# Kernel tuning notes

Hardware: AMD Instinct MI355X
Metric: run time of the kernel (lower is better)

## Reference

```python
import jax, jax.numpy as jnp
import numpy as np


def setup_inputs() -> dict:
    key = jax.random.key(0)
    k1, k2 = jax.random.split(key)
    B, H, S = 16, 512, 1024          # batch, hidden=nd*embed_dim, seqlen
    ND, ED, K = 4, 128, 4096         # nd, embed_dim, num_embed
    inputs = jax.random.normal(k1, (B, H, S), dtype=jnp.float32)
    embeddings = jax.random.normal(k2, (ND, ED, K), dtype=jnp.float32)
    return {"inputs": inputs, "embeddings": embeddings}


def reference(inputs, embeddings):
    # VectorQuant.forward with soft_train=False, gsoftmax=False, EMA=False (VQ-VAE straight-through path)
    commit_cost = 0.25
    B, H, S = inputs.shape
    ND, ED, K = embeddings.shape
    # stack_enc_outputs: (B, H, S) -> (B*S, nd, embed_dim) via contiguous view (C-order reshape)
    enc = inputs.reshape(B * S, ND, ED)
    x2 = jnp.sum(enc * enc, axis=2, keepdims=True)            # (BS, nd, 1)
    e2 = jnp.sum(embeddings * embeddings, axis=1)[None]       # (1, nd, K)
    cross = jnp.einsum('dhk,bdh->bdk', embeddings, enc)       # (BS, nd, K)
    distances = x2 + e2 - 2.0 * cross
    # per-token, per-chunk nearest code
    latents = jnp.argmin(distances, axis=2).T                 # (nd, BS)
    # gather codebook vectors: embeddings[d][:, latents[d]] -> (nd, ED, BS)
    encodings = jnp.take_along_axis(embeddings, latents[:, None, :], axis=2)
    # split_outputs: (nd, ED, B*S) -> (B, H, S) via contiguous view (C-order reshape)
    encodings = encodings.reshape(B, H, S)
    # straight-through estimator
    output = inputs + jax.lax.stop_gradient(encodings) - jax.lax.stop_gradient(inputs)
    commit_loss = jnp.mean((inputs - jax.lax.stop_gradient(encodings)) ** 2)
    loss = commit_cost * commit_loss
    kl = jnp.asarray(0, dtype=jnp.int32)
    return (output, loss, commit_loss, kl)
```

## Files before the change

kernel.cpp:

```cpp
#include <hip/hip_runtime.h>

#define ND 4
#define ED 128
#define KCODES 4096
#define NTOK 16384
#define HID 512
#define NTOT (ND*ED*NTOK)

#define MARGIN 2.0e-3f
#define FLAG_CAP 16384

typedef __attribute__((ext_vector_type(8))) short short8v;
typedef __attribute__((ext_vector_type(4))) float float4v;

#define GLDS16(g, l) __builtin_amdgcn_global_load_lds( \
    (const __attribute__((address_space(1))) unsigned int*)(g), \
    (__attribute__((address_space(3))) unsigned int*)(l), 16, 0, 0)

__device__ __forceinline__ unsigned short bf16h(float x) {
    unsigned u = __float_as_uint(x);
    return (unsigned short)((u + 0x7fffu + ((u >> 16) & 1u)) >> 16);
}
__device__ __forceinline__ float bf16f(unsigned short h) {
    return __uint_as_float(((unsigned)h) << 16);
}

__global__ __launch_bounds__(256) void e2split_kernel(const float* __restrict__ emb,
        float* __restrict__ e2g, unsigned short* __restrict__ bfrag,
        int* __restrict__ flag_cnt) {
    __shared__ float Tf[128][17];
    const int tile = blockIdx.x;
    const int d    = blockIdx.y;
    const int tid  = threadIdx.x;
    const int k0   = tile * 16;
    if (tile == 0 && d == 0 && tid == 0) *flag_cnt = 0;
    {
        int e = tid >> 1, half = tid & 1;
        const float* src = emb + ((size_t)d * ED + e) * KCODES + k0 + half * 8;
        float4 v0 = *(const float4*)(src);
        float4 v1 = *(const float4*)(src + 4);
        float* dst = &Tf[e][half * 8];
        dst[0] = v0.x; dst[1] = v0.y; dst[2] = v0.z; dst[3] = v0.w;
        dst[4] = v1.x; dst[5] = v1.y; dst[6] = v1.z; dst[7] = v1.w;
    }
    __syncthreads();
    if (tid < 16) {
        float s = 0.f;
        for (int e = 0; e < ED; ++e) {
            float v = Tf[e][tid];
            s = __fadd_rn(s, __fmul_rn(v, v));
        }
        e2g[d * KCODES + k0 + tid] = s;
    }
    #pragma unroll
    for (int q = 0; q < 2; ++q) {
        int c    = q * 256 + tid;
        int arr  = c >> 8;
        int rem  = c & 255;
        int code = rem >> 4;
        int kpos = rem & 15;
        int e0   = (kpos ^ code) * 8;
        short8v v;
        #pragma unroll
        for (int j = 0; j < 8; ++j) {
            float x = Tf[e0 + j][code];
            unsigned short hb = bf16h(x);
            v[j] = arr ? (short)bf16h(x - bf16f(hb)) : (short)hb;
        }
        size_t idx = ((size_t)(d * 256 + tile)) * 4096 + arr * 2048 + code * 128 + kpos * 8;
        *(short8v*)(bfrag + idx) = v;
    }
}

__global__ __launch_bounds__(256, 2)
void argmin_mfma_kernel(const float* __restrict__ in,
        const unsigned short* __restrict__ bfrag, const float* __restrict__ e2g,
        unsigned long long* __restrict__ pk, unsigned* __restrict__ pm2) {
    __shared__ __align__(16) char LB[40960];

    const int l   = blockIdx.x;
    const int r8  = l & 7;
    const int d   = r8 >> 1;
    const int h   = r8 & 1;
    const int tI  = l >> 3;
    const int t0  = tI * 128;

    const int tid  = threadIdx.x;
    const int w    = tid >> 6;
    const int lane = tid & 63;
    const int l15  = lane & 15;
    const int lk8  = lane >> 4;

    float* e2p = (float*)(LB + 32768);
    #pragma unroll
    for (int i = 0; i < 8; ++i) {
        int idx = i * 256 + tid;
        e2p[idx] = e2g[d * KCODES + h * 2048 + idx] + 512.0f;
    }

    short8v ahf[2][4], alf[2][4];
    #pragma unroll
    for (int rt = 0; rt < 2; ++rt) {
        const float* ap = in + (size_t)(t0 + w * 32 + rt * 16 + l15) * HID + d * ED + lk8 * 8;
        #pragma unroll
        for (int ks = 0; ks < 4; ++ks) {
            float4 v0 = *(const float4*)(ap + ks * 32);
            float4 v1 = *(const float4*)(ap + ks * 32 + 4);
            float vv[8] = {v0.x, v0.y, v0.z, v0.w, v1.x, v1.y, v1.z, v1.w};
            short8v hv, lv;
            #pragma unroll
            for (int j = 0; j < 8; ++j) {
                unsigned short hb = bf16h(vv[j]);
                hv[j] = (short)hb;
                lv[j] = (short)bf16h(vv[j] - bf16f(hb));
            }
            ahf[rt][ks] = hv; alf[rt][ks] = lv;
        }
    }

    int fo[4];
    #pragma unroll
    for (int ks = 0; ks < 4; ++ks)
        fo[ks] = l15 * 256 + (((ks * 4 + lk8) ^ l15) * 16);

    const char* sb = (const char*)bfrag + ((size_t)(d * 256 + h * 128)) * 8192 + tid * 16;

    #pragma unroll
    for (int t = 0; t < 3; ++t) {
        GLDS16(sb + t * 8192,        LB + t * 8192 + w * 1024);
        GLDS16(sb + t * 8192 + 4096, LB + t * 8192 + 4096 + w * 1024);
    }
    asm volatile("s_waitcnt vmcnt(2)" ::: "memory");
    __syncthreads();

    short8v rbh[4], rbl[4];
    #pragma unroll
    for (int ks = 0; ks < 4; ++ks) {
        rbh[ks] = *(const short8v*)(LB + fo[ks]);
        rbl[ks] = *(const short8v*)(LB + 4096 + fo[ks]);
    }

    unsigned m1[2][4], m2[2][4];
    int bk[2][4];
    #pragma unroll
    for (int rt = 0; rt < 2; ++rt)
        #pragma unroll
        for (int r = 0; r < 4; ++r) { m1[rt][r] = 0xFFFFFFFFu; m2[rt][r] = 0xFFFFFFFFu; bk[rt][r] = 0; }

    #pragma unroll 4
    for (int j = 0; j < 128; ++j) {
        if (j < 125) {
            const char* sp = sb + (size_t)(j + 3) * 8192;
            char* dp = LB + ((j + 3) & 3) * 8192 + w * 1024;
            GLDS16(sp,        dp);
            GLDS16(sp + 4096, dp + 4096);
        }
        const float e2v = e2p[j * 16 + l15];
        const char* nb = LB + ((j + 1) & 3) * 8192;

        float4v aP[2] = {{0,0,0,0},{0,0,0,0}};
        float4v aQ[2] = {{0,0,0,0},{0,0,0,0}};
        #define KSTEP(ks) \
            aP[0] = __builtin_amdgcn_mfma_f32_16x16x32_bf16(ahf[0][ks], rbh[ks], aP[0], 0, 0, 0); \
            aP[1] = __builtin_amdgcn_mfma_f32_16x16x32_bf16(ahf[1][ks], rbh[ks], aP[1], 0, 0, 0); \
            aP[0] = __builtin_amdgcn_mfma_f32_16x16x32_bf16(alf[0][ks], rbh[ks], aP[0], 0, 0, 0); \
            aP[1] = __builtin_amdgcn_mfma_f32_16x16x32_bf16(alf[1][ks], rbh[ks], aP[1], 0, 0, 0); \
            aQ[0] = __builtin_amdgcn_mfma_f32_16x16x32_bf16(ahf[0][ks], rbl[ks], aQ[0], 0, 0, 0); \
            aQ[1] = __builtin_amdgcn_mfma_f32_16x16x32_bf16(ahf[1][ks], rbl[ks], aQ[1], 0, 0, 0); \
            if (j < 127) { \
                rbh[ks] = *(const short8v*)(nb + fo[ks]); \
                rbl[ks] = *(const short8v*)(nb + 4096 + fo[ks]); \
            }
        KSTEP(0)
        KSTEP(1)
        KSTEP(2)
        KSTEP(3)
        #undef KSTEP

        #pragma unroll
        for (int rt = 0; rt < 2; ++rt) {
            #pragma unroll
            for (int r = 0; r < 4; ++r) {
                float cs = aP[rt][r] + aQ[rt][r];
                float dv = __fmaf_rn(-2.0f, cs, e2v);
                unsigned kk = __float_as_uint(dv);
                unsigned mo = m1[rt][r];
                unsigned mx = mo > kk ? mo : kk;
                m2[rt][r] = m2[rt][r] < mx ? m2[rt][r] : mx;
                if (kk < mo) { bk[rt][r] = j; m1[rt][r] = kk; }
            }
        }
        if (j < 124)  asm volatile("s_waitcnt vmcnt(2)" ::: "memory");
        else          asm volatile("s_waitcnt vmcnt(0)" ::: "memory");
        __builtin_amdgcn_s_barrier();
    }

    #pragma unroll
    for (int rt = 0; rt < 2; ++rt) {
        #pragma unroll
        for (int r = 0; r < 4; ++r) {
            unsigned long long key = ((unsigned long long)m1[rt][r] << 32) |
                                     (unsigned)(h * 2048 + bk[rt][r] * 16 + l15);
            unsigned mm2 = m2[rt][r];
            #pragma unroll
            for (int m = 1; m <= 8; m <<= 1) {
                unsigned long long ok = __shfl_xor(key, m, 64);
                unsigned om = __shfl_xor(mm2, m, 64);
                unsigned loser = (ok < key) ? (unsigned)(key >> 32) : (unsigned)(ok >> 32);
                key = ok < key ? ok : key;
                unsigned t2 = om < loser ? om : loser;
                mm2 = mm2 < t2 ? mm2 : t2;
            }
            if (l15 == 0) {
                int tok = d * NTOK + t0 + w * 32 + rt * 16 + lk8 * 4 + r;
                pk[(size_t)h * 65536 + tok] = key;
                pm2[(size_t)h * 65536 + tok] = mm2;
            }
        }
    }
}

__global__ __launch_bounds__(256) void merge_kernel(
        const unsigned long long* __restrict__ pk, const unsigned* __restrict__ pm2,
        int* __restrict__ lat, int* __restrict__ flag_cnt, int* __restrict__ flag_list) {
    int tok = blockIdx.x * 256 + threadIdx.x;
    unsigned long long ka = pk[tok], kb = pk[65536 + tok];
    unsigned m2a = pm2[tok], m2b = pm2[65536 + tok];
    bool aw = ka < kb;
    unsigned long long kw = aw ? ka : kb;
    unsigned loser1 = (unsigned)((aw ? kb : ka) >> 32);
    unsigned m2w = aw ? m2a : m2b;
    unsigned B2 = m2w < loser1 ? m2w : loser1;
    lat[tok] = (int)(kw & 0xFFFFu);
    float gap = __uint_as_float(B2) - __uint_as_float((unsigned)(kw >> 32));
    if (gap < MARGIN) {
        int slot = atomicAdd(flag_cnt, 1);
        if (slot < FLAG_CAP) flag_list[slot] = tok;
    }
}

__global__ __launch_bounds__(256) void repair_kernel(const float* __restrict__ in,
        const float* __restrict__ emb, const float* __restrict__ e2g,
        const int* __restrict__ flag_cnt, const int* __restrict__ flag_list,
        int* __restrict__ lat) {
    __shared__ float xs[ED];
    __shared__ float rd[256];
    __shared__ int   rk[256];
    int n = *flag_cnt;
    if (n > FLAG_CAP) n = FLAG_CAP;
    for (int idx = blockIdx.x; idx < n; idx += gridDim.x) {
        int tok = flag_list[idx];
        int d = tok >> 14;
        int t = tok & (NTOK - 1);
        __syncthreads();
        if (threadIdx.x < ED) xs[threadIdx.x] = in[(size_t)t * HID + d * ED + threadIdx.x];
        __syncthreads();
        float x2v = 0.f;
        for (int e = 0; e < ED; ++e) x2v = __fadd_rn(x2v, __fmul_rn(xs[e], xs[e]));
        const float* __restrict__ embd = emb + (size_t)d * ED * KCODES;
        float bd = 3.0e38f; int bkk = 0;
        for (int j = 0; j < 16; ++j) {
            int k = threadIdx.x + j * 256;
            float acc = 0.f;
            #pragma unroll 16
            for (int e = 0; e < ED; ++e)
                acc = __fmaf_rn(xs[e], embd[(size_t)e * KCODES + k], acc);
            float dist = __fsub_rn(__fadd_rn(x2v, e2g[d * KCODES + k]),
                                   __fmul_rn(2.0f, acc));
            if (dist < bd) { bd = dist; bkk = k; }
        }
        rd[threadIdx.x] = bd; rk[threadIdx.x] = bkk;
        __syncthreads();
        for (int w = 128; w > 0; w >>= 1) {
            if (threadIdx.x < w) {
                float od = rd[threadIdx.x + w]; int ok = rk[threadIdx.x + w];
                if (od < rd[threadIdx.x] || (od == rd[threadIdx.x] && ok < rk[threadIdx.x])) {
                    rd[threadIdx.x] = od; rk[threadIdx.x] = ok;
                }
            }
            __syncthreads();
        }
        if (threadIdx.x == 0) lat[tok] = rk[0];
    }
}

__global__ __launch_bounds__(256) void gather_kernel(const float* __restrict__ in,
        const float* __restrict__ emb, const int* __restrict__ lat,
        float* __restrict__ out, float* __restrict__ partial) {
    int tid  = threadIdx.x;
    int base = blockIdx.x * 1024 + tid * 4;
    int d = base >> 21;
    int e = (base >> 14) & 127;
    int t = base & (NTOK - 1);
    const int4 kk = *(const int4*)(lat + d * NTOK + t);
    const float* __restrict__ row = emb + ((size_t)(d * ED + e)) * KCODES;
    float enc[4];
    enc[0] = row[kk.x]; enc[1] = row[kk.y]; enc[2] = row[kk.z]; enc[3] = row[kk.w];
    const float4 x = *(const float4*)(in + base);
    const float xv[4] = {x.x, x.y, x.z, x.w};
    float4 ov; float* o = (float*)&ov;
    float s = 0.f;
    #pragma unroll
    for (int i = 0; i < 4; ++i) {
        o[i] = __fsub_rn(__fadd_rn(xv[i], enc[i]), xv[i]);
        float df = xv[i] - enc[i];
        s = __fmaf_rn(df, df, s);
    }
    *(float4*)(out + base) = ov;
    #pragma unroll
    for (int off = 32; off > 0; off >>= 1) s += __shfl_down(s, off, 64);
    __shared__ float wsum[4];
    if ((tid & 63) == 0) wsum[tid >> 6] = s;
    __syncthreads();
    if (tid == 0) partial[blockIdx.x] = wsum[0] + wsum[1] + wsum[2] + wsum[3];
}

__global__ __launch_bounds__(256) void finalize_kernel(const float* __restrict__ partial,
                                                       float* __restrict__ out_tail) {
    __shared__ double sh[256];
    double s = 0.0;
    for (int i = threadIdx.x; i < 8192; i += 256) s += (double)partial[i];
    sh[threadIdx.x] = s;
    __syncthreads();
    for (int w = 128; w > 0; w >>= 1) {
        if (threadIdx.x < w) sh[threadIdx.x] += sh[threadIdx.x + w];
        __syncthreads();
    }
    if (threadIdx.x == 0) {
        double mean = sh[0] / (double)NTOT;
        out_tail[0] = (float)(0.25 * mean);
        out_tail[1] = (float)mean;
        ((int*)out_tail)[2] = 0;
    }
}

extern "C" void kernel_launch(void* const* d_in, const int* in_sizes, int n_in,
                              void* d_out, int out_size, void* d_ws, size_t ws_size,
                              hipStream_t stream) {
    const float* in  = (const float*)d_in[0];
    const float* emb = (const float*)d_in[1];
    float* out = (float*)d_out;
    char* ws = (char*)d_ws;

    int*   lat       = (int*)ws;
    float* e2g       = (float*)(ws + 262144);
    float* partial   = (float*)(ws + 327680);
    int*   flag_cnt  = (int*)(ws + 360448);
    int*   flag_list = (int*)(ws + 360452);
    unsigned long long* pk  = (unsigned long long*)(ws + 458752);
    unsigned*           pm2 = (unsigned*)(ws + 1572864);
    unsigned short* bfrag = (unsigned short*)(ws + 2097152);

    hipLaunchKernelGGL(e2split_kernel, dim3(256, 4), dim3(256), 0, stream,
                       emb, e2g, bfrag, flag_cnt);
    hipLaunchKernelGGL(argmin_mfma_kernel, dim3(1024), dim3(256), 0, stream,
                       in, bfrag, e2g, pk, pm2);
    hipLaunchKernelGGL(merge_kernel, dim3(256), dim3(256), 0, stream,
                       pk, pm2, lat, flag_cnt, flag_list);
    hipLaunchKernelGGL(repair_kernel, dim3(64), dim3(256), 0, stream,
                       in, emb, e2g, flag_cnt, flag_list, lat);
    hipLaunchKernelGGL(gather_kernel, dim3(NTOT / 1024), dim3(256), 0, stream,
                       in, emb, lat, out, partial);
    hipLaunchKernelGGL(finalize_kernel, dim3(1), dim3(256), 0, stream, partial, out + NTOT);
}
```

Measured before the change: 273.8 us.

## Give each wave a private double-buffered codebook stream, removing per-iteration block barriers

Each wave now loads the full 16KB codebook tile into its own LDS region (double-buffered) instead of sharing a 4-stage buffer across the block. This removes the block-wide s_barrier every iteration, so waves synchronise only on their own vmcnt/lgkmcnt counters. The cost is four times as much global-to-LDS traffic per block and larger LDS use (72KB), which may lower occupancy below the two blocks per CU the launch bounds request. The min tracking also switches from unsigned bit comparisons to float fmin/fmax.

```diff
diff --git a/kernel.cpp b/kernel.cpp
--- a/kernel.cpp
+++ b/kernel.cpp
@@ -76,7 +76,7 @@
 void argmin_mfma_kernel(const float* __restrict__ in,
         const unsigned short* __restrict__ bfrag, const float* __restrict__ e2g,
         unsigned long long* __restrict__ pk, unsigned* __restrict__ pm2) {
-    __shared__ __align__(16) char LB[40960];
+    __shared__ __align__(16) char LB[73728];
 
     const int l   = blockIdx.x;
     const int r8  = l & 7;
@@ -91,12 +91,13 @@
     const int l15  = lane & 15;
     const int lk8  = lane >> 4;
 
-    float* e2p = (float*)(LB + 32768);
+    float* e2p = (float*)(LB + 65536);
     #pragma unroll
     for (int i = 0; i < 8; ++i) {
         int idx = i * 256 + tid;
         e2p[idx] = e2g[d * KCODES + h * 2048 + idx] + 512.0f;
     }
+    __syncthreads();
 
     short8v ahf[2][4], alf[2][4];
     #pragma unroll
@@ -123,40 +124,44 @@
     for (int ks = 0; ks < 4; ++ks)
         fo[ks] = l15 * 256 + (((ks * 4 + lk8) ^ l15) * 16);
 
-    const char* sb = (const char*)bfrag + ((size_t)(d * 256 + h * 128)) * 8192 + tid * 16;
-
-    #pragma unroll
-    for (int t = 0; t < 3; ++t) {
-        GLDS16(sb + t * 8192,        LB + t * 8192 + w * 1024);
-        GLDS16(sb + t * 8192 + 4096, LB + t * 8192 + 4096 + w * 1024);
-    }
-    asm volatile("s_waitcnt vmcnt(2)" ::: "memory");
-    __syncthreads();
+    const char* srec = (const char*)bfrag + ((size_t)(d * 256 + h * 128)) * 8192;
+    char* mybuf = LB + w * 16384;
+
+    #pragma unroll
+    for (int q = 0; q < 8; ++q) GLDS16(srec + q * 1024 + lane * 16, mybuf + q * 1024);
+    #pragma unroll
+    for (int q = 0; q < 8; ++q) GLDS16(srec + 8192 + q * 1024 + lane * 16,
+                                       mybuf + 8192 + q * 1024);
+    asm volatile("s_waitcnt vmcnt(8)" ::: "memory");
 
     short8v rbh[4], rbl[4];
     #pragma unroll
     for (int ks = 0; ks < 4; ++ks) {
-        rbh[ks] = *(const short8v*)(LB + fo[ks]);
-        rbl[ks] = *(const short8v*)(LB + 4096 + fo[ks]);
-    }
-
-    unsigned m1[2][4], m2[2][4];
+        rbh[ks] = *(const short8v*)(mybuf + fo[ks]);
+        rbl[ks] = *(const short8v*)(mybuf + 4096 + fo[ks]);
+    }
+
+    float m1[2][4], m2[2][4];
     int bk[2][4];
     #pragma unroll
     for (int rt = 0; rt < 2; ++rt)
         #pragma unroll
-        for (int r = 0; r < 4; ++r) { m1[rt][r] = 0xFFFFFFFFu; m2[rt][r] = 0xFFFFFFFFu; bk[rt][r] = 0; }
-
-    #pragma unroll 4
+        for (int r = 0; r < 4; ++r) { m1[rt][r] = 3.0e38f; m2[rt][r] = 3.0e38f; bk[rt][r] = 0; }
+
+    #pragma unroll 2
     for (int j = 0; j < 128; ++j) {
-        if (j < 125) {
-            const char* sp = sb + (size_t)(j + 3) * 8192;
-            char* dp = LB + ((j + 3) & 3) * 8192 + w * 1024;
-            GLDS16(sp,        dp);
-            GLDS16(sp + 4096, dp + 4096);
+        if (j < 126) {
+            asm volatile("s_waitcnt lgkmcnt(0)" ::: "memory");
+            const char* sp = srec + (size_t)(j + 2) * 8192;
+            char* dp = mybuf + (j & 1) * 8192;
+            #pragma unroll
+            for (int q = 0; q < 8; ++q) GLDS16(sp + q * 1024 + lane * 16, dp + q * 1024);
+            asm volatile("s_waitcnt vmcnt(8)" ::: "memory");
+        } else {
+            asm volatile("s_waitcnt vmcnt(0)" ::: "memory");
         }
         const float e2v = e2p[j * 16 + l15];
-        const char* nb = LB + ((j + 1) & 3) * 8192;
+        const char* nb = mybuf + ((j + 1) & 1) * 8192;
 
         float4v aP[2] = {{0,0,0,0},{0,0,0,0}};
         float4v aQ[2] = {{0,0,0,0},{0,0,0,0}};
@@ -183,25 +188,19 @@
             for (int r = 0; r < 4; ++r) {
                 float cs = aP[rt][r] + aQ[rt][r];
                 float dv = __fmaf_rn(-2.0f, cs, e2v);
-                unsigned kk = __float_as_uint(dv);
-                unsigned mo = m1[rt][r];
-                unsigned mx = mo > kk ? mo : kk;
-                m2[rt][r] = m2[rt][r] < mx ? m2[rt][r] : mx;
-                if (kk < mo) { bk[rt][r] = j; m1[rt][r] = kk; }
-            }
-        }
-        if (j < 124)  asm volatile("s_waitcnt vmcnt(2)" ::: "memory");
-        else          asm volatile("s_waitcnt vmcnt(0)" ::: "memory");
-        __builtin_amdgcn_s_barrier();
+                m2[rt][r] = fminf(fmaxf(dv, m1[rt][r]), m2[rt][r]);
+                if (dv < m1[rt][r]) { bk[rt][r] = j; m1[rt][r] = dv; }
+            }
+        }
     }
 
     #pragma unroll
     for (int rt = 0; rt < 2; ++rt) {
         #pragma unroll
         for (int r = 0; r < 4; ++r) {
-            unsigned long long key = ((unsigned long long)m1[rt][r] << 32) |
+            unsigned long long key = ((unsigned long long)__float_as_uint(m1[rt][r]) << 32) |
                                      (unsigned)(h * 2048 + bk[rt][r] * 16 + l15);
-            unsigned mm2 = m2[rt][r];
+            unsigned mm2 = __float_as_uint(m2[rt][r]);
             #pragma unroll
             for (int m = 1; m <= 8; m <<= 1) {
                 unsigned long long ok = __shfl_xor(key, m, 64);
```

New measurement: 310.7 us. 1.13x slower.
